# Optimization experiments

Hardware: AMD Instinct MI355X
Metric: run time of the kernel (lower is better)

Reference implementation:

```python
import jax, jax.numpy as jnp
import numpy as np

CODEBOOK_SIZE = 1024
EMBED_DIM = 64
COMMITMENT_COST = 0.25


def setup_inputs() -> dict:
    key = jax.random.key(0)
    k1, k2 = jax.random.split(key)
    z = jax.random.normal(k1, (8, EMBED_DIM, 8192), dtype=jnp.float32)
    # torch init: uniform(-1/codebook_size, 1/codebook_size)
    codebook_weight = jax.random.uniform(
        k2, (CODEBOOK_SIZE, EMBED_DIM), dtype=jnp.float32,
        minval=-1.0 / CODEBOOK_SIZE, maxval=1.0 / CODEBOOK_SIZE)
    return {"z": z, "codebook_weight": codebook_weight}


def reference(z, codebook_weight):
    B, D, T = z.shape
    # [B*T, D]
    z_flat = jnp.transpose(z, (0, 2, 1)).reshape(-1, D)
    # squared euclidean distances to each code: ||z||^2 - 2 z.W^T + ||W||^2
    distances = (jnp.sum(z_flat * z_flat, axis=1, keepdims=True)
                 - 2.0 * z_flat @ codebook_weight.T
                 + jnp.sum(codebook_weight * codebook_weight, axis=1))
    codes = jnp.argmin(distances, axis=1)  # [B*T]
    z_q = codebook_weight[codes].reshape(B, T, D).transpose(0, 2, 1)  # [B, D, T]
    commitment_loss = jnp.mean((jax.lax.stop_gradient(z_q) - z) ** 2)
    codebook_loss = jnp.mean((z_q - jax.lax.stop_gradient(z)) ** 2)
    vq_loss = codebook_loss + COMMITMENT_COST * commitment_loss
    # straight-through estimator
    z_q_st = z + jax.lax.stop_gradient(z_q - z)
    return z_q_st, vq_loss, codes
```

## Files before the change

### kernel.cpp

```cpp
#include <hip/hip_runtime.h>


#define T_DIM 8192
#define D_DIM 64
#define C_DIM 1024
#define B_DIM 8
#define NROWS (B_DIM * T_DIM)
#define NELEM (B_DIM * D_DIM * T_DIM)
#define SEGS 4
#define CODES_PER_SEG (C_DIM / SEGS)
#define EPI_BLOCKS (NELEM / 4 / 256)

#define R64(M) M(0) M(1) M(2) M(3) M(4) M(5) M(6) M(7) \
  M(8) M(9) M(10) M(11) M(12) M(13) M(14) M(15) \
  M(16) M(17) M(18) M(19) M(20) M(21) M(22) M(23) \
  M(24) M(25) M(26) M(27) M(28) M(29) M(30) M(31) \
  M(32) M(33) M(34) M(35) M(36) M(37) M(38) M(39) \
  M(40) M(41) M(42) M(43) M(44) M(45) M(46) M(47) \
  M(48) M(49) M(50) M(51) M(52) M(53) M(54) M(55) \
  M(56) M(57) M(58) M(59) M(60) M(61) M(62) M(63)

#define SQ_(x) __fmul_rn(x, x)
#define AD_(a, b) __fadd_rn(a, b)

#define PAIRWISE64(p, dst) \
  float pr0 = SQ_(p##0);  pr0 = AD_(pr0, SQ_(p##8));  pr0 = AD_(pr0, SQ_(p##16)); pr0 = AD_(pr0, SQ_(p##24)); pr0 = AD_(pr0, SQ_(p##32)); pr0 = AD_(pr0, SQ_(p##40)); pr0 = AD_(pr0, SQ_(p##48)); pr0 = AD_(pr0, SQ_(p##56)); \
  float pr1 = SQ_(p##1);  pr1 = AD_(pr1, SQ_(p##9));  pr1 = AD_(pr1, SQ_(p##17)); pr1 = AD_(pr1, SQ_(p##25)); pr1 = AD_(pr1, SQ_(p##33)); pr1 = AD_(pr1, SQ_(p##41)); pr1 = AD_(pr1, SQ_(p##49)); pr1 = AD_(pr1, SQ_(p##57)); \
  float pr2 = SQ_(p##2);  pr2 = AD_(pr2, SQ_(p##10)); pr2 = AD_(pr2, SQ_(p##18)); pr2 = AD_(pr2, SQ_(p##26)); pr2 = AD_(pr2, SQ_(p##34)); pr2 = AD_(pr2, SQ_(p##42)); pr2 = AD_(pr2, SQ_(p##50)); pr2 = AD_(pr2, SQ_(p##58)); \
  float pr3 = SQ_(p##3);  pr3 = AD_(pr3, SQ_(p##11)); pr3 = AD_(pr3, SQ_(p##19)); pr3 = AD_(pr3, SQ_(p##27)); pr3 = AD_(pr3, SQ_(p##35)); pr3 = AD_(pr3, SQ_(p##43)); pr3 = AD_(pr3, SQ_(p##51)); pr3 = AD_(pr3, SQ_(p##59)); \
  float pr4 = SQ_(p##4);  pr4 = AD_(pr4, SQ_(p##12)); pr4 = AD_(pr4, SQ_(p##20)); pr4 = AD_(pr4, SQ_(p##28)); pr4 = AD_(pr4, SQ_(p##36)); pr4 = AD_(pr4, SQ_(p##44)); pr4 = AD_(pr4, SQ_(p##52)); pr4 = AD_(pr4, SQ_(p##60)); \
  float pr5 = SQ_(p##5);  pr5 = AD_(pr5, SQ_(p##13)); pr5 = AD_(pr5, SQ_(p##21)); pr5 = AD_(pr5, SQ_(p##29)); pr5 = AD_(pr5, SQ_(p##37)); pr5 = AD_(pr5, SQ_(p##45)); pr5 = AD_(pr5, SQ_(p##53)); pr5 = AD_(pr5, SQ_(p##61)); \
  float pr6 = SQ_(p##6);  pr6 = AD_(pr6, SQ_(p##14)); pr6 = AD_(pr6, SQ_(p##22)); pr6 = AD_(pr6, SQ_(p##30)); pr6 = AD_(pr6, SQ_(p##38)); pr6 = AD_(pr6, SQ_(p##46)); pr6 = AD_(pr6, SQ_(p##54)); pr6 = AD_(pr6, SQ_(p##62)); \
  float pr7 = SQ_(p##7);  pr7 = AD_(pr7, SQ_(p##15)); pr7 = AD_(pr7, SQ_(p##23)); pr7 = AD_(pr7, SQ_(p##31)); pr7 = AD_(pr7, SQ_(p##39)); pr7 = AD_(pr7, SQ_(p##47)); pr7 = AD_(pr7, SQ_(p##55)); pr7 = AD_(pr7, SQ_(p##63)); \
  float dst = AD_(AD_(AD_(pr0, pr1), AD_(pr2, pr3)), AD_(AD_(pr4, pr5), AD_(pr6, pr7)));

__global__ __launch_bounds__(256, 4)
void vq_dist_kernel(const float* __restrict__ z,
                    const float* __restrict__ cb,
                    float2* __restrict__ pairs) {
    const int row = blockIdx.x * 256 + threadIdx.x;
    const int seg = blockIdx.y;
    const int c0 = seg * CODES_PER_SEG;
    const int b = row >> 13;
    const int t = row & (T_DIM - 1);

    __shared__ float wsqs[CODES_PER_SEG];
    {
        const float* wp = cb + ((size_t)(c0 + threadIdx.x) << 6);
#define LOADW(k) float w##k = wp[k];
        R64(LOADW)
#undef LOADW
        PAIRWISE64(w, s)
        wsqs[threadIdx.x] = s;
    }
    __syncthreads();

    const float* zp = z + (size_t)b * (D_DIM * T_DIM) + t;
#define LOADZ(k) float z##k = zp[(size_t)k * T_DIM]; \
                 asm volatile("" : "+v"(z##k));
    R64(LOADZ)
#undef LOADZ

    PAIRWISE64(z, zsq)

    float bestd = 3.4e38f;
    int besti = 0;
#pragma unroll 1
    for (int cc = 0; cc < CODES_PER_SEG; cc += 4) {
        const float* wpa = cb + ((size_t)(c0 + cc) << 6);
        const float* wpb = wpa + 64;
        const float* wpc = wpa + 128;
        const float* wpd = wpa + 192;
        float a0 = 0.f, a1 = 0.f, a2 = 0.f, a3 = 0.f;
#define DOT4(k) a0 = fmaf(z##k, wpa[k], a0); \
                a1 = fmaf(z##k, wpb[k], a1); \
                a2 = fmaf(z##k, wpc[k], a2); \
                a3 = fmaf(z##k, wpd[k], a3);
        R64(DOT4)
#undef DOT4
        float d0 = __fadd_rn(__fsub_rn(zsq, __fmul_rn(2.0f, a0)), wsqs[cc + 0]);
        float d1 = __fadd_rn(__fsub_rn(zsq, __fmul_rn(2.0f, a1)), wsqs[cc + 1]);
        float d2 = __fadd_rn(__fsub_rn(zsq, __fmul_rn(2.0f, a2)), wsqs[cc + 2]);
        float d3 = __fadd_rn(__fsub_rn(zsq, __fmul_rn(2.0f, a3)), wsqs[cc + 3]);
        if (d0 < bestd) { bestd = d0; besti = c0 + cc + 0; }
        if (d1 < bestd) { bestd = d1; besti = c0 + cc + 1; }
        if (d2 < bestd) { bestd = d2; besti = c0 + cc + 2; }
        if (d3 < bestd) { bestd = d3; besti = c0 + cc + 3; }
    }
    pairs[seg * NROWS + row] = make_float2(bestd, (float)besti);
}

__global__ void vq_argmin_kernel(const float2* __restrict__ pairs,
                                 float* __restrict__ codes) {
    int row = blockIdx.x * blockDim.x + threadIdx.x;
    float2 best = pairs[row];
#pragma unroll
    for (int s = 1; s < SEGS; ++s) {
        float2 p = pairs[s * NROWS + row];
        if (p.x < best.x) best = p;
    }
    codes[row] = best.y;
}

__global__ void vq_epilogue_kernel(const float* __restrict__ z,
                                   const float* __restrict__ cb,
                                   const float* __restrict__ codes,
                                   float* __restrict__ out,
                                   double* __restrict__ partials) {
    const int q = blockIdx.x * 256 + threadIdx.x;
    const int i = q << 2;
    const int t = i & (T_DIM - 1);
    const int bd = i >> 13;
    const int d = bd & (D_DIM - 1);
    const int b = bd >> 6;
    const int row = (b << 13) | t;

    float4 cr = *(const float4*)(codes + row);
    float4 zv = *(const float4*)(z + i);
    float w0 = cb[((int)cr.x << 6) + d];
    float w1 = cb[((int)cr.y << 6) + d];
    float w2 = cb[((int)cr.z << 6) + d];
    float w3 = cb[((int)cr.w << 6) + d];

    float4 df = make_float4(w0 - zv.x, w1 - zv.y, w2 - zv.z, w3 - zv.w);
    float4 o = make_float4(zv.x + df.x, zv.y + df.y, zv.z + df.z, zv.w + df.w);
    *(float4*)(out + i) = o;

    double v = (double)df.x * df.x + (double)df.y * df.y +
               (double)df.z * df.z + (double)df.w * df.w;
#pragma unroll
    for (int o2 = 32; o2 > 0; o2 >>= 1) v += __shfl_down(v, o2, 64);

    __shared__ double red[4];
    if ((threadIdx.x & 63) == 0) red[threadIdx.x >> 6] = v;
    __syncthreads();
    if (threadIdx.x == 0)
        partials[blockIdx.x] = ((red[0] + red[1]) + (red[2] + red[3]));
}

__global__ void vq_loss_kernel(const double* __restrict__ partials,
                               float* __restrict__ out_loss) {
    double s = 0.0;
    for (int i = threadIdx.x; i < EPI_BLOCKS; i += 256) s += partials[i];
#pragma unroll
    for (int o = 32; o > 0; o >>= 1) s += __shfl_down(s, o, 64);
    __shared__ double red[4];
    if ((threadIdx.x & 63) == 0) red[threadIdx.x >> 6] = s;
    __syncthreads();
    if (threadIdx.x == 0) {
        double tot = (red[0] + red[1]) + (red[2] + red[3]);
        out_loss[0] = (float)(1.25 * tot / (double)NELEM);
    }
}

extern "C" void kernel_launch(void* const* d_in, const int* in_sizes, int n_in,
                              void* d_out, int out_size, void* d_ws, size_t ws_size,
                              hipStream_t stream) {
    const float* z  = (const float*)d_in[0];
    const float* cb = (const float*)d_in[1];

    float* out      = (float*)d_out;
    float* out_loss = out + NELEM;
    float* codes    = out + NELEM + 1;

    char* ws    = (char*)d_ws;
    double* partials = (double*)(ws);
    float2* pairs = (float2*)(ws + 32768);

    dim3 grid1(NROWS / 256, SEGS);
    vq_dist_kernel<<<grid1, 256, 0, stream>>>(z, cb, pairs);

    vq_argmin_kernel<<<NROWS / 256, 256, 0, stream>>>(pairs, codes);

    vq_epilogue_kernel<<<EPI_BLOCKS, 256, 0, stream>>>(z, cb, codes, out, partials);

    vq_loss_kernel<<<1, 256, 0, stream>>>(partials, out_loss);
}
```

Baseline: 262.6 us.

## Stage z rows in LDS and compute eight codes per distance-loop iteration

The distance kernel no longer holds all 64 z values per row in registers. Each thread writes its row into padded shared memory (stride 65) and reads it back inside the code loop. That register saving pays for eight accumulators per iteration instead of four, halving the number of loop passes, and the block size drops to 128. An opaque scalar zero offset is added, likely to stop the compiler from hoisting the LDS reads back into registers. The risk is extra LDS traffic, one z read shared by eight FMAs per k, against better occupancy and more reuse of each z load.

```diff
diff --git a/kernel.cpp b/kernel.cpp
--- a/kernel.cpp
+++ b/kernel.cpp
@@ -9,6 +9,8 @@
 #define NELEM (B_DIM * D_DIM * T_DIM)
 #define SEGS 4
 #define CODES_PER_SEG (C_DIM / SEGS)
+#define BLK 128
+#define ZSTRIDE 65
 #define EPI_BLOCKS (NELEM / 4 / 256)
 
 #define R64(M) M(0) M(1) M(2) M(3) M(4) M(5) M(6) M(7) \
@@ -34,58 +36,90 @@
   float pr7 = SQ_(p##7);  pr7 = AD_(pr7, SQ_(p##15)); pr7 = AD_(pr7, SQ_(p##23)); pr7 = AD_(pr7, SQ_(p##31)); pr7 = AD_(pr7, SQ_(p##39)); pr7 = AD_(pr7, SQ_(p##47)); pr7 = AD_(pr7, SQ_(p##55)); pr7 = AD_(pr7, SQ_(p##63)); \
   float dst = AD_(AD_(AD_(pr0, pr1), AD_(pr2, pr3)), AD_(AD_(pr4, pr5), AD_(pr6, pr7)));
 
-__global__ __launch_bounds__(256, 4)
+__global__ __launch_bounds__(BLK)
 void vq_dist_kernel(const float* __restrict__ z,
                     const float* __restrict__ cb,
                     float2* __restrict__ pairs) {
-    const int row = blockIdx.x * 256 + threadIdx.x;
+    __shared__ float z_lds[BLK * ZSTRIDE];
+    __shared__ float wsqs[CODES_PER_SEG];
+
+    const int tid = threadIdx.x;
+    const int row = blockIdx.x * BLK + tid;
     const int seg = blockIdx.y;
     const int c0 = seg * CODES_PER_SEG;
     const int b = row >> 13;
     const int t = row & (T_DIM - 1);
 
-    __shared__ float wsqs[CODES_PER_SEG];
-    {
-        const float* wp = cb + ((size_t)(c0 + threadIdx.x) << 6);
+    for (int cc = tid; cc < CODES_PER_SEG; cc += BLK) {
+        const float* wp = cb + ((size_t)(c0 + cc) << 6);
 #define LOADW(k) float w##k = wp[k];
         R64(LOADW)
 #undef LOADW
         PAIRWISE64(w, s)
-        wsqs[threadIdx.x] = s;
-    }
+        wsqs[cc] = s;
+    }
+
+    const float* zp = z + (size_t)b * (D_DIM * T_DIM) + t;
+    float col[8];
+#pragma unroll
+    for (int d = 0; d < 8; ++d) {
+        float v = zp[(size_t)d * T_DIM];
+        z_lds[tid * ZSTRIDE + d] = v;
+        col[d] = __fmul_rn(v, v);
+    }
+#pragma unroll
+    for (int d = 8; d < 64; ++d) {
+        float v = zp[(size_t)d * T_DIM];
+        z_lds[tid * ZSTRIDE + d] = v;
+        col[d & 7] = __fadd_rn(col[d & 7], __fmul_rn(v, v));
+    }
+    const float zsq = __fadd_rn(
+        __fadd_rn(__fadd_rn(col[0], col[1]), __fadd_rn(col[2], col[3])),
+        __fadd_rn(__fadd_rn(col[4], col[5]), __fadd_rn(col[6], col[7])));
     __syncthreads();
 
-    const float* zp = z + (size_t)b * (D_DIM * T_DIM) + t;
-#define LOADZ(k) float z##k = zp[(size_t)k * T_DIM]; \
-                 asm volatile("" : "+v"(z##k));
-    R64(LOADZ)
-#undef LOADZ
-
-    PAIRWISE64(z, zsq)
-
+    const float* zbase = z_lds + tid * ZSTRIDE;
     float bestd = 3.4e38f;
     int besti = 0;
 #pragma unroll 1
-    for (int cc = 0; cc < CODES_PER_SEG; cc += 4) {
-        const float* wpa = cb + ((size_t)(c0 + cc) << 6);
-        const float* wpb = wpa + 64;
-        const float* wpc = wpa + 128;
-        const float* wpd = wpa + 192;
+    for (int cc = 0; cc < CODES_PER_SEG; cc += 8) {
+        int zoff;
+        asm volatile("s_mov_b32 %0, 0" : "=s"(zoff));
+        const float* zl = zbase + zoff;
+
+        const float* w0p = cb + ((size_t)(c0 + cc) << 6);
+        const float* w1p = w0p + 64;
+        const float* w2p = w0p + 128;
+        const float* w3p = w0p + 192;
+        const float* w4p = w0p + 256;
+        const float* w5p = w0p + 320;
+        const float* w6p = w0p + 384;
+        const float* w7p = w0p + 448;
         float a0 = 0.f, a1 = 0.f, a2 = 0.f, a3 = 0.f;
-#define DOT4(k) a0 = fmaf(z##k, wpa[k], a0); \
-                a1 = fmaf(z##k, wpb[k], a1); \
-                a2 = fmaf(z##k, wpc[k], a2); \
-                a3 = fmaf(z##k, wpd[k], a3);
-        R64(DOT4)
-#undef DOT4
+        float a4 = 0.f, a5 = 0.f, a6 = 0.f, a7 = 0.f;
+#define STEP(k) { float zv = zl[k]; \
+        a0 = fmaf(zv, w0p[k], a0); a1 = fmaf(zv, w1p[k], a1); \
+        a2 = fmaf(zv, w2p[k], a2); a3 = fmaf(zv, w3p[k], a3); \
+        a4 = fmaf(zv, w4p[k], a4); a5 = fmaf(zv, w5p[k], a5); \
+        a6 = fmaf(zv, w6p[k], a6); a7 = fmaf(zv, w7p[k], a7); }
+        R64(STEP)
+#undef STEP
         float d0 = __fadd_rn(__fsub_rn(zsq, __fmul_rn(2.0f, a0)), wsqs[cc + 0]);
         float d1 = __fadd_rn(__fsub_rn(zsq, __fmul_rn(2.0f, a1)), wsqs[cc + 1]);
         float d2 = __fadd_rn(__fsub_rn(zsq, __fmul_rn(2.0f, a2)), wsqs[cc + 2]);
         float d3 = __fadd_rn(__fsub_rn(zsq, __fmul_rn(2.0f, a3)), wsqs[cc + 3]);
+        float d4 = __fadd_rn(__fsub_rn(zsq, __fmul_rn(2.0f, a4)), wsqs[cc + 4]);
+        float d5 = __fadd_rn(__fsub_rn(zsq, __fmul_rn(2.0f, a5)), wsqs[cc + 5]);
+        float d6 = __fadd_rn(__fsub_rn(zsq, __fmul_rn(2.0f, a6)), wsqs[cc + 6]);
+        float d7 = __fadd_rn(__fsub_rn(zsq, __fmul_rn(2.0f, a7)), wsqs[cc + 7]);
         if (d0 < bestd) { bestd = d0; besti = c0 + cc + 0; }
         if (d1 < bestd) { bestd = d1; besti = c0 + cc + 1; }
         if (d2 < bestd) { bestd = d2; besti = c0 + cc + 2; }
         if (d3 < bestd) { bestd = d3; besti = c0 + cc + 3; }
+        if (d4 < bestd) { bestd = d4; besti = c0 + cc + 4; }
+        if (d5 < bestd) { bestd = d5; besti = c0 + cc + 5; }
+        if (d6 < bestd) { bestd = d6; besti = c0 + cc + 6; }
+        if (d7 < bestd) { bestd = d7; besti = c0 + cc + 7; }
     }
     pairs[seg * NROWS + row] = make_float2(bestd, (float)besti);
 }
@@ -167,8 +201,8 @@
     double* partials = (double*)(ws);
     float2* pairs = (float2*)(ws + 32768);
 
-    dim3 grid1(NROWS / 256, SEGS);
-    vq_dist_kernel<<<grid1, 256, 0, stream>>>(z, cb, pairs);
+    dim3 grid1(NROWS / BLK, SEGS);
+    vq_dist_kernel<<<grid1, BLK, 0, stream>>>(z, cb, pairs);
 
     vq_argmin_kernel<<<NROWS / 256, 256, 0, stream>>>(pairs, codes);
 
```

Measured after the change: 303.5 us. +15.6%, slower.
